# Kernel tuning notes

Hardware: AMD Instinct MI355X
Metric: run time of the kernel (lower is better)

Reference implementation:

```python
import jax, jax.numpy as jnp
import numpy as np

LEVELS = [(100, 128), (50, 64), (25, 32), (13, 16), (7, 8)]
B, C, S = 16, 80, 17064  # batch, class_num, sum(h*w)
GAMMA, ALPHA = 2.0, 0.25


def setup_inputs() -> dict:
    key = jax.random.key(0)
    ks = iter(jax.random.split(key, 40))
    inp = {}
    for i, (h, w) in enumerate(LEVELS):
        inp[f"cls_p{i}"] = jax.random.normal(next(ks), (B, C, h, w), dtype=jnp.float32)
        inp[f"cnt_p{i}"] = jax.random.normal(next(ks), (B, 1, h, w), dtype=jnp.float32)
        inp[f"reg_p{i}"] = jax.random.uniform(next(ks), (B, 4, h, w), dtype=jnp.float32) * 8.0 + 0.1
    keep = jax.random.uniform(next(ks), (B, S, 1)) > 0.7
    cnt_val = jax.random.uniform(next(ks), (B, S, 1), dtype=jnp.float32)
    inp["cnt_targets"] = jnp.where(keep, cnt_val, -1.0)
    inp["reg_targets"] = jax.random.uniform(next(ks), (B, S, 4), dtype=jnp.float32) * 8.0 + 0.1
    inp["cls_targets"] = jax.random.randint(next(ks), (B, S, 1), 0, 81, dtype=jnp.int64)
    return inp


def _flatten_levels(preds, c):
    # each pred [B,c,h,w] -> [B,h*w,c]; concat over levels -> [B,S,c]
    return jnp.concatenate(
        [p.transpose(0, 2, 3, 1).reshape(p.shape[0], -1, c) for p in preds], axis=1)


def _fcos_loss(cls_ps, cnt_ps, reg_ps, cls_t, cnt_t, reg_t):
    mask = (cnt_t > -1.0)[..., 0]                       # [B,S] bool positive mask
    num_pos = jnp.clip(jnp.sum(mask, axis=1), 1).astype(jnp.float32)  # [B]

    # ---- focal cls loss (over ALL locations, as in the original) ----
    cls = _flatten_levels(cls_ps, C)                    # [B,S,C]
    onehot = (jnp.arange(1, C + 1)[None, None, :] == cls_t).astype(jnp.float32)
    p = jax.nn.sigmoid(cls)
    p_t = onehot * p + (1.0 - onehot) * (1.0 - p)
    alpha_f = onehot * ALPHA + (1.0 - onehot) * (1.0 - ALPHA)
    focal = -alpha_f * (1.0 - p_t) ** GAMMA * jnp.log(p_t)
    cls_loss = jnp.mean(jnp.sum(focal, axis=(1, 2)) / num_pos)

    # ---- centerness BCE-with-logits, masked sum ----
    cnt = _flatten_levels(cnt_ps, 1)[..., 0]            # [B,S]
    t = cnt_t[..., 0]
    bce = jnp.maximum(cnt, 0.0) - cnt * t + jnp.log1p(jnp.exp(-jnp.abs(cnt)))
    cnt_loss = jnp.mean(jnp.sum(bce * mask, axis=1) / num_pos)

    # ---- GIoU reg loss, masked sum ----
    reg = _flatten_levels(reg_ps, 4)                    # [B,S,4] ltrb offsets
    lt_min = jnp.minimum(reg[..., :2], reg_t[..., :2])
    rb_min = jnp.minimum(reg[..., 2:], reg_t[..., 2:])
    wh_min = jnp.clip(rb_min + lt_min, 0.0)
    overlap = wh_min[..., 0] * wh_min[..., 1]
    area1 = (reg[..., 2] + reg[..., 0]) * (reg[..., 3] + reg[..., 1])
    area2 = (reg_t[..., 2] + reg_t[..., 0]) * (reg_t[..., 3] + reg_t[..., 1])
    union = area1 + area2 - overlap
    iou = overlap / union
    lt_max = jnp.maximum(reg[..., :2], reg_t[..., :2])
    rb_max = jnp.maximum(reg[..., 2:], reg_t[..., 2:])
    wh_max = jnp.clip(rb_max + lt_max, 0.0)
    g_area = wh_max[..., 0] * wh_max[..., 1]
    giou = iou - (g_area - union) / jnp.clip(g_area, 1e-10)
    reg_loss = jnp.mean(jnp.sum((1.0 - giou) * mask, axis=1) / num_pos)

    total = cls_loss + cnt_loss + reg_loss  # add_centerness=True
    return (cls_loss, cnt_loss, reg_loss, total)


def reference(cls_p0, cls_p1, cls_p2, cls_p3, cls_p4,
              cnt_p0, cnt_p1, cnt_p2, cnt_p3, cnt_p4,
              reg_p0, reg_p1, reg_p2, reg_p3, reg_p4,
              cnt_targets, reg_targets, cls_targets):
    return _fcos_loss([cls_p0, cls_p1, cls_p2, cls_p3, cls_p4],
                      [cnt_p0, cnt_p1, cnt_p2, cnt_p3, cnt_p4],
                      [reg_p0, reg_p1, reg_p2, reg_p3, reg_p4],
                      cls_targets, cnt_targets, reg_targets)
```

## Files before the change

### kernel.cpp

```cpp
#include <hip/hip_runtime.h>

#define S_TOTAL 17064
#define NB 16
#define NC 80
#define QPB 4266
#define NXQ 17
#define NJ 7
#define TOTAL_BLOCKS (NB * NJ * NXQ)
#define PL TOTAL_BLOCKS

typedef float vfloat4 __attribute__((ext_vector_type(4)));

struct Ptrs {
    const float* cls[5];
    const float* cnt[5];
    const float* reg[5];
    const float* cnt_t;
    const float* reg_t;
    const int*   cls_t;
    float*       ws;
    float*       out;
};

__device__ __forceinline__ float focal_term(float x, bool o) {
    const float xs = o ? x : -x;
    const float af = o ? 0.25f : 0.75f;
    const float em = __expf(-xs);
    const float pt = 1.0f / (1.0f + em);
    const float q  = em * pt;
    return af * q * q * __logf(1.0f + em);
}

__device__ __forceinline__ float giou_term(float pl, float pt_, float pr, float pb,
                                           float tl, float tt, float tr, float tb) {
    const float overlap = fmaxf(fminf(pr, tr) + fminf(pl, tl), 0.0f) *
                          fmaxf(fminf(pb, tb) + fminf(pt_, tt), 0.0f);
    const float area1 = (pr + pl) * (pb + pt_);
    const float area2 = (tr + tl) * (tb + tt);
    const float uni = area1 + area2 - overlap;
    const float iou = overlap / uni;
    const float ga = fmaxf(fmaxf(pr, tr) + fmaxf(pl, tl), 0.0f) *
                     fmaxf(fmaxf(pb, tb) + fmaxf(pt_, tt), 0.0f);
    const float giou = iou - (ga - uni) / fmaxf(ga, 1e-10f);
    return 1.0f - giou;
}

__device__ __forceinline__ float bce_term(float x, float t) {
    return fmaxf(x, 0.0f) - x * t + __logf(1.0f + __expf(-fabsf(x)));
}

__global__ __launch_bounds__(256) void fcos_main(Ptrs p) {
    const int bid = (int)blockIdx.x;
    const int b   = bid / (NJ * NXQ);
    const int r   = bid - b * (NJ * NXQ);
    const int j   = r / NXQ;
    const int xq  = r - j * NXQ;
    const int fq  = xq * 256 + (int)threadIdx.x;

    int lvl, qb, hw, off;
    if (fq < 3200)      { lvl = 0; qb = 0;    hw = 12800; off = 0;     }
    else if (fq < 4000) { lvl = 1; qb = 3200; hw = 3200;  off = 12800; }
    else if (fq < 4200) { lvl = 2; qb = 4000; hw = 800;   off = 16000; }
    else if (fq < 4252) { lvl = 3; qb = 4200; hw = 208;   off = 16800; }
    else                { lvl = 4; qb = 4252; hw = 56;    off = 17008; }
    const bool active = (fq < QPB);

    float acls = 0.f, acnt = 0.f, areg = 0.f, apos = 0.f;

    if (active) {
        const int s0  = (fq - qb) << 2;
        const int gs0 = b * S_TOTAL + off + s0;
        const int4 tq = *(const int4*)(p.cls_t + gs0);

        const int cbase = j * 12;
        const int ncls  = (j < 6) ? 12 : 8;
        const float* cp = p.cls[lvl] + (size_t)((b * NC + cbase) * hw + s0);

        float a0 = 0.f, a1 = 0.f, a2 = 0.f, a3 = 0.f;
        #pragma unroll 4
        for (int c = 0; c < ncls; ++c) {
            const vfloat4 v = *(const vfloat4*)(cp + (size_t)(c * hw));
            const int c1 = cbase + c + 1;
            a0 += focal_term(v.x, tq.x == c1);
            a1 += focal_term(v.y, tq.y == c1);
            a2 += focal_term(v.z, tq.z == c1);
            a3 += focal_term(v.w, tq.w == c1);
        }
        acls = (a0 + a1) + (a2 + a3);

        if (j == 6) {
            const float4 tC  = *(const float4*)(p.cnt_t + gs0);
            const float4 xc  = *(const float4*)(p.cnt[lvl] + (size_t)(b * hw + s0));
            const float m0 = (tC.x > -1.0f) ? 1.0f : 0.0f;
            const float m1 = (tC.y > -1.0f) ? 1.0f : 0.0f;
            const float m2 = (tC.z > -1.0f) ? 1.0f : 0.0f;
            const float m3 = (tC.w > -1.0f) ? 1.0f : 0.0f;
            apos = m0 + m1 + m2 + m3;
            acnt = bce_term(xc.x, tC.x) * m0 + bce_term(xc.y, tC.y) * m1 +
                   bce_term(xc.z, tC.z) * m2 + bce_term(xc.w, tC.w) * m3;

            const float* rp  = p.reg[lvl] + (size_t)(b * 4 * hw + s0);
            const float4 pl  = *(const float4*)(rp);
            const float4 pt_ = *(const float4*)(rp + (size_t)hw);
            const float4 pr  = *(const float4*)(rp + (size_t)(2 * hw));
            const float4 pb  = *(const float4*)(rp + (size_t)(3 * hw));
            const float4 t0  = *(const float4*)(p.reg_t + (size_t)(gs0 + 0) * 4);
            const float4 t1  = *(const float4*)(p.reg_t + (size_t)(gs0 + 1) * 4);
            const float4 t2  = *(const float4*)(p.reg_t + (size_t)(gs0 + 2) * 4);
            const float4 t3  = *(const float4*)(p.reg_t + (size_t)(gs0 + 3) * 4);

            areg = giou_term(pl.x, pt_.x, pr.x, pb.x, t0.x, t0.y, t0.z, t0.w) * m0 +
                   giou_term(pl.y, pt_.y, pr.y, pb.y, t1.x, t1.y, t1.z, t1.w) * m1 +
                   giou_term(pl.z, pt_.z, pr.z, pb.z, t2.x, t2.y, t2.z, t2.w) * m2 +
                   giou_term(pl.w, pt_.w, pr.w, pb.w, t3.x, t3.y, t3.z, t3.w) * m3;
        }
    }

    #pragma unroll
    for (int d = 32; d; d >>= 1) {
        acls += __shfl_down(acls, d);
        acnt += __shfl_down(acnt, d);
        areg += __shfl_down(areg, d);
        apos += __shfl_down(apos, d);
    }

    __shared__ float red[4][4];
    const int wave = threadIdx.x >> 6;
    const int lane = threadIdx.x & 63;
    if (lane == 0) {
        red[0][wave] = acls;
        red[1][wave] = acnt;
        red[2][wave] = areg;
        red[3][wave] = apos;
    }
    __syncthreads();
    if (threadIdx.x == 0) {
        p.ws[bid]          = red[0][0] + red[0][1] + red[0][2] + red[0][3];
        p.ws[PL + bid]     = red[1][0] + red[1][1] + red[1][2] + red[1][3];
        p.ws[2 * PL + bid] = red[2][0] + red[2][1] + red[2][2] + red[2][3];
        p.ws[3 * PL + bid] = red[3][0] + red[3][1] + red[3][2] + red[3][3];
    }
}

__global__ __launch_bounds__(256) void fcos_finalize(const float* __restrict__ ws,
                                                     float* __restrict__ out) {
    __shared__ float s[4][256];
    __shared__ float lb[3][NB];
    const int t = (int)threadIdx.x;
    const int b = t >> 4;
    const int k = t & 15;

    float q0 = 0.f, q1 = 0.f, q2 = 0.f, q3 = 0.f;
    for (int i = k; i < NJ * NXQ; i += 16) {
        const int slot = b * (NJ * NXQ) + i;
        q0 += ws[slot];
        q1 += ws[PL + slot];
        q2 += ws[2 * PL + slot];
        q3 += ws[3 * PL + slot];
    }
    s[0][t] = q0; s[1][t] = q1; s[2][t] = q2; s[3][t] = q3;
    __syncthreads();

    if (t < NB) {
        float cls = 0.f, cnt = 0.f, reg = 0.f, pos = 0.f;
        #pragma unroll
        for (int kk = 0; kk < 16; ++kk) {
            cls += s[0][t * 16 + kk];
            cnt += s[1][t * 16 + kk];
            reg += s[2][t * 16 + kk];
            pos += s[3][t * 16 + kk];
        }
        const float np = fmaxf(pos, 1.0f);
        lb[0][t] = cls / np;
        lb[1][t] = cnt / np;
        lb[2][t] = reg / np;
    }
    __syncthreads();

    if (t == 0) {
        float l0 = 0.f, l1 = 0.f, l2 = 0.f;
        #pragma unroll
        for (int bb = 0; bb < NB; ++bb) {
            l0 += lb[0][bb]; l1 += lb[1][bb]; l2 += lb[2][bb];
        }
        l0 *= (1.0f / NB); l1 *= (1.0f / NB); l2 *= (1.0f / NB);
        out[0] = l0;
        out[1] = l1;
        out[2] = l2;
        out[3] = l0 + l1 + l2;
    }
}

extern "C" void kernel_launch(void* const* d_in, const int* in_sizes, int n_in,
                              void* d_out, int out_size, void* d_ws, size_t ws_size,
                              hipStream_t stream) {
    Ptrs p;
    for (int i = 0; i < 5; ++i) {
        p.cls[i] = (const float*)d_in[3 * i + 0];
        p.cnt[i] = (const float*)d_in[3 * i + 1];
        p.reg[i] = (const float*)d_in[3 * i + 2];
    }
    p.cnt_t = (const float*)d_in[15];
    p.reg_t = (const float*)d_in[16];
    p.cls_t = (const int*)  d_in[17];
    p.ws    = (float*)d_ws;
    p.out   = (float*)d_out;

    fcos_main<<<dim3(TOTAL_BLOCKS), 256, 0, stream>>>(p);
    fcos_finalize<<<dim3(1), 256, 0, stream>>>((const float*)d_ws, (float*)d_out);
}
```

Measured before the change: 149.1 us.

## Split focal loss into dense negative sum plus sparse positive correction

Computes the focal loss for every class logit as if all were negatives, streaming each level's cls tensor contiguously in a separate kernel. A second kernel adds a per-location correction (positive term minus negative term) only at the target class, and also computes the centerness and GIoU terms. This removes the per-element class comparison and lets the dominant read be fully contiguous. The cost is an extra kernel launch and a scattered gather of one logit per positive location.

```diff
diff --git a/kernel.cpp b/kernel.cpp
--- a/kernel.cpp
+++ b/kernel.cpp
@@ -5,9 +5,11 @@
 #define NC 80
 #define QPB 4266
 #define NXQ 17
-#define NJ 7
-#define TOTAL_BLOCKS (NB * NJ * NXQ)
-#define PL TOTAL_BLOCKS
+
+#define NA_BLOCKS 2064
+#define SLOTS_PER_B 129
+#define WSB 2064
+#define NBXQ (NB * NXQ)
 
 typedef float vfloat4 __attribute__((ext_vector_type(4)));
 
@@ -49,12 +51,48 @@
     return fmaxf(x, 0.0f) - x * t + __logf(1.0f + __expf(-fabsf(x)));
 }
 
-__global__ __launch_bounds__(256) void fcos_main(Ptrs p) {
+__global__ __launch_bounds__(256) void fcos_neg(Ptrs p) {
+    const int bx = (int)blockIdx.x;
+
+    int lvl, b, cnk, slot, CH, TOT;
+    if (bx < 1536)      { lvl = 0; b = bx / 96;  cnk = bx - 96 * b;
+                          slot = cnk;        CH = 2667; TOT = 256000; }
+    else if (bx < 1920) { const int r = bx - 1536; lvl = 1; b = r / 24; cnk = r - 24 * b;
+                          slot = 96 + cnk;   CH = 2667; TOT = 64000; }
+    else if (bx < 2016) { const int r = bx - 1920; lvl = 2; b = r / 6;  cnk = r - 6 * b;
+                          slot = 120 + cnk;  CH = 2667; TOT = 16000; }
+    else if (bx < 2048) { const int r = bx - 2016; lvl = 3; b = r >> 1; cnk = r & 1;
+                          slot = 126 + cnk;  CH = 2080; TOT = 4160; }
+    else                { const int r = bx - 2048; lvl = 4; b = r;      cnk = 0;
+                          slot = 128;        CH = 1120; TOT = 1120; }
+
+    const vfloat4* bp = (const vfloat4*)(p.cls[lvl] + (size_t)b * 4 * TOT);
+    const int i0   = cnk * CH;
+    const int iend = min(i0 + CH, TOT);
+
+    float acc = 0.f;
+    #pragma unroll 2
+    for (int i = i0 + (int)threadIdx.x; i < iend; i += 256) {
+        const vfloat4 v = bp[i];
+        acc += (focal_term(v.x, false) + focal_term(v.y, false)) +
+               (focal_term(v.z, false) + focal_term(v.w, false));
+    }
+
+    #pragma unroll
+    for (int d = 32; d; d >>= 1) acc += __shfl_down(acc, d);
+
+    __shared__ float red[4];
+    const int wave = threadIdx.x >> 6;
+    if ((threadIdx.x & 63) == 0) red[wave] = acc;
+    __syncthreads();
+    if (threadIdx.x == 0)
+        p.ws[b * SLOTS_PER_B + slot] = (red[0] + red[1]) + (red[2] + red[3]);
+}
+
+__global__ __launch_bounds__(256) void fcos_pos(Ptrs p) {
     const int bid = (int)blockIdx.x;
-    const int b   = bid / (NJ * NXQ);
-    const int r   = bid - b * (NJ * NXQ);
-    const int j   = r / NXQ;
-    const int xq  = r - j * NXQ;
+    const int b   = bid / NXQ;
+    const int xq  = bid - b * NXQ;
     const int fq  = xq * 256 + (int)threadIdx.x;
 
     int lvl, qb, hw, off;
@@ -65,60 +103,52 @@
     else                { lvl = 4; qb = 4252; hw = 56;    off = 17008; }
     const bool active = (fq < QPB);
 
-    float acls = 0.f, acnt = 0.f, areg = 0.f, apos = 0.f;
+    float corr = 0.f, acnt = 0.f, areg = 0.f, apos = 0.f;
 
     if (active) {
         const int s0  = (fq - qb) << 2;
         const int gs0 = b * S_TOTAL + off + s0;
         const int4 tq = *(const int4*)(p.cls_t + gs0);
-
-        const int cbase = j * 12;
-        const int ncls  = (j < 6) ? 12 : 8;
-        const float* cp = p.cls[lvl] + (size_t)((b * NC + cbase) * hw + s0);
-
-        float a0 = 0.f, a1 = 0.f, a2 = 0.f, a3 = 0.f;
-        #pragma unroll 4
-        for (int c = 0; c < ncls; ++c) {
-            const vfloat4 v = *(const vfloat4*)(cp + (size_t)(c * hw));
-            const int c1 = cbase + c + 1;
-            a0 += focal_term(v.x, tq.x == c1);
-            a1 += focal_term(v.y, tq.y == c1);
-            a2 += focal_term(v.z, tq.z == c1);
-            a3 += focal_term(v.w, tq.w == c1);
+        const float* cb = p.cls[lvl] + (size_t)(b * NC) * hw + s0;
+
+        #pragma unroll
+        for (int e = 0; e < 4; ++e) {
+            const int ti = (e == 0) ? tq.x : (e == 1) ? tq.y : (e == 2) ? tq.z : tq.w;
+            if (ti > 0) {
+                const float x = cb[(size_t)(ti - 1) * hw + e];
+                corr += focal_term(x, true) - focal_term(x, false);
+            }
         }
-        acls = (a0 + a1) + (a2 + a3);
-
-        if (j == 6) {
-            const float4 tC  = *(const float4*)(p.cnt_t + gs0);
-            const float4 xc  = *(const float4*)(p.cnt[lvl] + (size_t)(b * hw + s0));
-            const float m0 = (tC.x > -1.0f) ? 1.0f : 0.0f;
-            const float m1 = (tC.y > -1.0f) ? 1.0f : 0.0f;
-            const float m2 = (tC.z > -1.0f) ? 1.0f : 0.0f;
-            const float m3 = (tC.w > -1.0f) ? 1.0f : 0.0f;
-            apos = m0 + m1 + m2 + m3;
-            acnt = bce_term(xc.x, tC.x) * m0 + bce_term(xc.y, tC.y) * m1 +
-                   bce_term(xc.z, tC.z) * m2 + bce_term(xc.w, tC.w) * m3;
-
-            const float* rp  = p.reg[lvl] + (size_t)(b * 4 * hw + s0);
-            const float4 pl  = *(const float4*)(rp);
-            const float4 pt_ = *(const float4*)(rp + (size_t)hw);
-            const float4 pr  = *(const float4*)(rp + (size_t)(2 * hw));
-            const float4 pb  = *(const float4*)(rp + (size_t)(3 * hw));
-            const float4 t0  = *(const float4*)(p.reg_t + (size_t)(gs0 + 0) * 4);
-            const float4 t1  = *(const float4*)(p.reg_t + (size_t)(gs0 + 1) * 4);
-            const float4 t2  = *(const float4*)(p.reg_t + (size_t)(gs0 + 2) * 4);
-            const float4 t3  = *(const float4*)(p.reg_t + (size_t)(gs0 + 3) * 4);
-
-            areg = giou_term(pl.x, pt_.x, pr.x, pb.x, t0.x, t0.y, t0.z, t0.w) * m0 +
-                   giou_term(pl.y, pt_.y, pr.y, pb.y, t1.x, t1.y, t1.z, t1.w) * m1 +
-                   giou_term(pl.z, pt_.z, pr.z, pb.z, t2.x, t2.y, t2.z, t2.w) * m2 +
-                   giou_term(pl.w, pt_.w, pr.w, pb.w, t3.x, t3.y, t3.z, t3.w) * m3;
-        }
+
+        const float4 tC  = *(const float4*)(p.cnt_t + gs0);
+        const float4 xc  = *(const float4*)(p.cnt[lvl] + (size_t)(b * hw + s0));
+        const float m0 = (tC.x > -1.0f) ? 1.0f : 0.0f;
+        const float m1 = (tC.y > -1.0f) ? 1.0f : 0.0f;
+        const float m2 = (tC.z > -1.0f) ? 1.0f : 0.0f;
+        const float m3 = (tC.w > -1.0f) ? 1.0f : 0.0f;
+        apos = m0 + m1 + m2 + m3;
+        acnt = bce_term(xc.x, tC.x) * m0 + bce_term(xc.y, tC.y) * m1 +
+               bce_term(xc.z, tC.z) * m2 + bce_term(xc.w, tC.w) * m3;
+
+        const float* rp  = p.reg[lvl] + (size_t)(b * 4 * hw + s0);
+        const float4 pl  = *(const float4*)(rp);
+        const float4 pt_ = *(const float4*)(rp + (size_t)hw);
+        const float4 pr  = *(const float4*)(rp + (size_t)(2 * hw));
+        const float4 pb  = *(const float4*)(rp + (size_t)(3 * hw));
+        const float4 t0  = *(const float4*)(p.reg_t + (size_t)(gs0 + 0) * 4);
+        const float4 t1  = *(const float4*)(p.reg_t + (size_t)(gs0 + 1) * 4);
+        const float4 t2  = *(const float4*)(p.reg_t + (size_t)(gs0 + 2) * 4);
+        const float4 t3  = *(const float4*)(p.reg_t + (size_t)(gs0 + 3) * 4);
+
+        areg = giou_term(pl.x, pt_.x, pr.x, pb.x, t0.x, t0.y, t0.z, t0.w) * m0 +
+               giou_term(pl.y, pt_.y, pr.y, pb.y, t1.x, t1.y, t1.z, t1.w) * m1 +
+               giou_term(pl.z, pt_.z, pr.z, pb.z, t2.x, t2.y, t2.z, t2.w) * m2 +
+               giou_term(pl.w, pt_.w, pr.w, pb.w, t3.x, t3.y, t3.z, t3.w) * m3;
     }
 
     #pragma unroll
     for (int d = 32; d; d >>= 1) {
-        acls += __shfl_down(acls, d);
+        corr += __shfl_down(corr, d);
         acnt += __shfl_down(acnt, d);
         areg += __shfl_down(areg, d);
         apos += __shfl_down(apos, d);
@@ -128,17 +158,16 @@
     const int wave = threadIdx.x >> 6;
     const int lane = threadIdx.x & 63;
     if (lane == 0) {
-        red[0][wave] = acls;
-        red[1][wave] = acnt;
-        red[2][wave] = areg;
-        red[3][wave] = apos;
+        red[0][wave] = corr; red[1][wave] = acnt;
+        red[2][wave] = areg; red[3][wave] = apos;
     }
     __syncthreads();
     if (threadIdx.x == 0) {
-        p.ws[bid]          = red[0][0] + red[0][1] + red[0][2] + red[0][3];
-        p.ws[PL + bid]     = red[1][0] + red[1][1] + red[1][2] + red[1][3];
-        p.ws[2 * PL + bid] = red[2][0] + red[2][1] + red[2][2] + red[2][3];
-        p.ws[3 * PL + bid] = red[3][0] + red[3][1] + red[3][2] + red[3][3];
+        const int s = b * NXQ + xq;
+        p.ws[WSB + 0 * NBXQ + s] = red[0][0] + red[0][1] + red[0][2] + red[0][3];
+        p.ws[WSB + 1 * NBXQ + s] = red[1][0] + red[1][1] + red[1][2] + red[1][3];
+        p.ws[WSB + 2 * NBXQ + s] = red[2][0] + red[2][1] + red[2][2] + red[2][3];
+        p.ws[WSB + 3 * NBXQ + s] = red[3][0] + red[3][1] + red[3][2] + red[3][3];
     }
 }
 
@@ -150,15 +179,17 @@
     const int b = t >> 4;
     const int k = t & 15;
 
-    float q0 = 0.f, q1 = 0.f, q2 = 0.f, q3 = 0.f;
-    for (int i = k; i < NJ * NXQ; i += 16) {
-        const int slot = b * (NJ * NXQ) + i;
-        q0 += ws[slot];
-        q1 += ws[PL + slot];
-        q2 += ws[2 * PL + slot];
-        q3 += ws[3 * PL + slot];
-    }
-    s[0][t] = q0; s[1][t] = q1; s[2][t] = q2; s[3][t] = q3;
+    float qc = 0.f;
+    for (int i = k; i < SLOTS_PER_B; i += 16) qc += ws[b * SLOTS_PER_B + i];
+    float q1 = 0.f, q2 = 0.f, q3 = 0.f;
+    for (int i = k; i < NXQ; i += 16) {
+        const int sl = b * NXQ + i;
+        qc += ws[WSB + 0 * NBXQ + sl];
+        q1 += ws[WSB + 1 * NBXQ + sl];
+        q2 += ws[WSB + 2 * NBXQ + sl];
+        q3 += ws[WSB + 3 * NBXQ + sl];
+    }
+    s[0][t] = qc; s[1][t] = q1; s[2][t] = q2; s[3][t] = q3;
     __syncthreads();
 
     if (t < NB) {
@@ -206,6 +237,7 @@
     p.ws    = (float*)d_ws;
     p.out   = (float*)d_out;
 
-    fcos_main<<<dim3(TOTAL_BLOCKS), 256, 0, stream>>>(p);
+    fcos_neg<<<dim3(NA_BLOCKS), 256, 0, stream>>>(p);
+    fcos_pos<<<dim3(NBXQ), 256, 0, stream>>>(p);
     fcos_finalize<<<dim3(1), 256, 0, stream>>>((const float*)d_ws, (float*)d_out);
 }
```

Result: slower. 161.3 us (+8.2%).
